# Kernel tuning notes

Measured on AMD Instinct MI355X. Metric: run time of the kernel, lower is better.

Reference implementation:

```python
import jax, jax.numpy as jnp
import numpy as np

B, D, H, E, K, A = 65536, 44, 256, 4, 2, 8  # batch, state_dim, hidden, experts, top_k, action_dim


def setup_inputs() -> dict:
    key = jax.random.key(0)
    ks = jax.random.split(key, 10)
    s = 0.1  # weight scale
    return dict(
        state=jax.random.normal(ks[0], (B, D), dtype=jnp.float32),
        rW1=jax.random.normal(ks[1], (D, H // 2)) * s, rb1=jnp.zeros((H // 2,)),
        rW2=jax.random.normal(ks[2], (H // 2, E)) * s, rb2=jnp.zeros((E,)),
        eW1=jax.random.normal(ks[3], (E, D, H)) * s, eb1=jnp.zeros((E, H)),
        eg1=jnp.ones((E, H)), ebt1=jnp.zeros((E, H)),
        eW2=jax.random.normal(ks[4], (E, H, H)) * s, eb2=jnp.zeros((E, H)),
        eg2=jnp.ones((E, H)), ebt2=jnp.zeros((E, H)),
        eW3=jax.random.normal(ks[5], (E, H, 2 * A)) * s, eb3=jnp.zeros((E, 2 * A)),
        vW1=jax.random.normal(ks[6], (D, H)) * s, vb1=jnp.zeros((H,)),
        vg=jnp.ones((H,)), vbt=jnp.zeros((H,)),
        vW2=jax.random.normal(ks[7], (H, H // 2)) * s, vb2=jnp.zeros((H // 2,)),
        vW3=jax.random.normal(ks[8], (H // 2, 1)) * s, vb3=jnp.zeros((1,)),
    )


def _ln(x, g, b):
    m = jnp.mean(x, axis=-1, keepdims=True)
    v = jnp.mean(jnp.square(x - m), axis=-1, keepdims=True)
    return (x - m) * jax.lax.rsqrt(v + 1e-5) * g + b


def reference(state, rW1, rb1, rW2, rb2,
              eW1, eb1, eg1, ebt1, eW2, eb2, eg2, ebt2, eW3, eb3,
              vW1, vb1, vg, vbt, vW2, vb2, vW3, vb3):
    # Router (eval mode: no noise)
    h = jax.nn.relu(state @ rW1 + rb1)
    router_probs = jax.nn.softmax(h @ rW2 + rb2, axis=-1)          # [B, E]
    top_v, top_i = jax.lax.top_k(router_probs, K)                  # [B, K]
    top_v = top_v / (jnp.sum(top_v, axis=-1, keepdims=True) + 1e-8)
    # Dense combine weights per expert (equivalent to per-sample gather/scatter loop)
    combine = jnp.sum(jax.nn.one_hot(top_i, E, dtype=state.dtype) * top_v[..., None], axis=1)  # [B, E]

    def expert(W1, b1, g1, bt1, W2, b2, g2, bt2, W3, b3):
        y = jax.nn.relu(_ln(state @ W1 + b1, g1, bt1))   # [B, H]
        y = jax.nn.relu(_ln(y @ W2 + b2, g2, bt2))       # [B, H]
        return y @ W3 + b3                               # [B, 2A]

    eout = jax.vmap(expert)(eW1, eb1, eg1, ebt1, eW2, eb2, eg2, ebt2, eW3, eb3)  # [E, B, 2A]
    mix = jnp.einsum('ebd,be->bd', eout, combine)        # [B, 2A]

    alpha = jax.nn.softplus(mix[:, :A]) + 1.0
    beta = jax.nn.softplus(mix[:, A:]) + 1.0

    v = jax.nn.relu(_ln(state @ vW1 + vb1, vg, vbt))
    v = jax.nn.relu(v @ vW2 + vb2)
    value = v @ vW3 + vb3                                # [B, 1]
    return alpha, beta, value, router_probs
```

## Files before the change

kernel.cpp:

```cpp
#include <hip/hip_runtime.h>
#include <math.h>

#define NB 65536

using f32x4 = __attribute__((ext_vector_type(4))) float;
using u32x4 = __attribute__((ext_vector_type(4))) unsigned;
using bf16x8 = __attribute__((ext_vector_type(8))) __bf16;

__device__ __forceinline__ unsigned pk2(float lo, float hi) {
    return (unsigned)__builtin_bit_cast(unsigned short, (__bf16)lo)
         | ((unsigned)__builtin_bit_cast(unsigned short, (__bf16)hi) << 16);
}
__device__ __forceinline__ float softplus_f(float x) {
    return fmaxf(x, 0.f) + log1pf(expf(-fabsf(x)));
}

#define MFMA16(acc, a, b) acc = __builtin_amdgcn_mfma_f32_16x16x32_bf16(a, b, acc, 0, 0, 0)

__device__ __forceinline__ bf16x8 cvt8(f32x4 a, f32x4 b) {
    union { bf16x8 v; unsigned u[4]; } r;
    r.u[0] = pk2(a[0], a[1]); r.u[1] = pk2(a[2], a[3]);
    r.u[2] = pk2(b[0], b[1]); r.u[3] = pk2(b[2], b[3]);
    return r.v;
}

__device__ __forceinline__ const bf16x8* ys_frag(const unsigned short* ys, int row, int col) {
    return (const bf16x8*)&ys[row * 256 + (col ^ ((row & 7) << 3))];
}

template<int NJ>
__device__ __forceinline__ void ldch(f32x4* r, const f32x4* __restrict__ src, int tid) {
    #pragma unroll
    for (int j = 0; j < NJ; ++j) r[j] = src[tid + j * 256];
}
template<int NJ>
__device__ __forceinline__ void wrch(unsigned short* buf, const f32x4* r, int tid) {
    #pragma unroll
    for (int j = 0; j < NJ; ++j) *(f32x4*)&buf[(size_t)(tid + j * 256) * 8] = r[j];
}

template<int NT>
__device__ __forceinline__ void mfma_bcols(f32x4* acc, bf16x8 a, const unsigned short* bufp, int c, int g) {
    #pragma unroll
    for (int t = 0; t < NT; ++t) {
        bf16x8 b = *(const bf16x8*)&bufp[t * 512 + g * 128 + c * 8];
        MFMA16(acc[t], a, b);
    }
}

__device__ __forceinline__ void ln_relu_store(
    f32x4* acc, const float* bs, const float* gs, const float* ts,
    unsigned int* ysu, int stripe, int g, int c)
{
    #pragma unroll
    for (int t = 0; t < 16; ++t) {
        float bb = bs[t * 16 + c];
        #pragma unroll
        for (int r = 0; r < 4; ++r) acc[t][r] += bb;
    }
    float sum[4] = {0.f, 0.f, 0.f, 0.f}, sq[4] = {0.f, 0.f, 0.f, 0.f};
    #pragma unroll
    for (int t = 0; t < 16; ++t) {
        #pragma unroll
        for (int r = 0; r < 4; ++r) { sum[r] += acc[t][r]; sq[r] += acc[t][r] * acc[t][r]; }
    }
    #pragma unroll
    for (int m = 1; m < 16; m <<= 1) {
        #pragma unroll
        for (int r = 0; r < 4; ++r) { sum[r] += __shfl_xor(sum[r], m); sq[r] += __shfl_xor(sq[r], m); }
    }
    float rs[4], nm[4];
    #pragma unroll
    for (int r = 0; r < 4; ++r) {
        float mean = sum[r] * (1.f / 256.f);
        float var = sq[r] * (1.f / 256.f) - mean * mean;
        rs[r] = rsqrtf(var + 1e-5f);
        nm[r] = -mean * rs[r];
    }
    const int odd = c & 1;
    const int ra = stripe + g * 4 + (odd ? 2 : 0);
    const int sza = (ra & 7) << 2, szb = ((ra + 1) & 7) << 2;
    #pragma unroll
    for (int t = 0; t < 16; ++t) {
        float gg = gs[t * 16 + c], bb = ts[t * 16 + c];
        float v0 = fmaxf(fmaf(fmaf(acc[t][0], rs[0], nm[0]), gg, bb), 0.f);
        float v1 = fmaxf(fmaf(fmaf(acc[t][1], rs[1], nm[1]), gg, bb), 0.f);
        float v2 = fmaxf(fmaf(fmaf(acc[t][2], rs[2], nm[2]), gg, bb), 0.f);
        float v3 = fmaxf(fmaf(fmaf(acc[t][3], rs[3], nm[3]), gg, bb), 0.f);
        float o0 = __shfl_xor(v0, 1), o1 = __shfl_xor(v1, 1);
        float o2 = __shfl_xor(v2, 1), o3 = __shfl_xor(v3, 1);
        unsigned p0 = pk2(odd ? o0 : v0, odd ? v0 : o0);
        unsigned p1 = pk2(odd ? o1 : v1, odd ? v1 : o1);
        unsigned p2 = pk2(odd ? o2 : v2, odd ? v2 : o2);
        unsigned p3 = pk2(odd ? o3 : v3, odd ? v3 : o3);
        unsigned pa = odd ? p2 : p0;
        unsigned pb = odd ? p3 : p1;
        int cp = t * 8 + (c >> 1);
        ysu[ra * 128 + (cp ^ sza)] = pa;
        ysu[(ra + 1) * 128 + (cp ^ szb)] = pb;
    }
}

__global__ __launch_bounds__(256) void k1_prep(
    const float* __restrict__ eW1, const float* __restrict__ eW2, const float* __restrict__ eW3,
    const float* __restrict__ vW1, const float* __restrict__ vW2,
    unsigned int* __restrict__ w1img, unsigned int* __restrict__ w2img,
    unsigned int* __restrict__ vw1img, unsigned int* __restrict__ vw2img,
    unsigned int* __restrict__ w3img)
{
    int fid = blockIdx.x * 256 + threadIdx.x;
    float v[8];
    unsigned int* dst;
    if (fid < 8192) {
        int e = fid >> 11, ch = (fid >> 10) & 1, rr = fid & 1023;
        int t = rr >> 6, g = (rr >> 4) & 3, c = rr & 15;
        int h = t * 16 + c, k0 = ch * 32 + g * 8;
        #pragma unroll
        for (int j = 0; j < 8; ++j) {
            int k = k0 + j;
            v[j] = (k < 44) ? eW1[(e * 44 + k) * 256 + h] : 0.f;
        }
        dst = w1img + (size_t)fid * 4;
    } else if (fid < 40960) {
        int f = fid - 8192;
        int e = f >> 13, ch = (f >> 10) & 7, rr = f & 1023;
        int t = rr >> 6, g = (rr >> 4) & 3, c = rr & 15;
        int h = t * 16 + c, k0 = ch * 32 + g * 8;
        const float* base = eW2 + (size_t)e * 65536 + h;
        #pragma unroll
        for (int j = 0; j < 8; ++j) v[j] = base[(size_t)(k0 + j) * 256];
        dst = w2img + (size_t)f * 4;
    } else if (fid < 43008) {
        int f = fid - 40960;
        int ch = f >> 10, rr = f & 1023;
        int t = rr >> 6, g = (rr >> 4) & 3, c = rr & 15;
        int h = t * 16 + c, k0 = ch * 32 + g * 8;
        #pragma unroll
        for (int j = 0; j < 8; ++j) {
            int k = k0 + j;
            v[j] = (k < 44) ? vW1[k * 256 + h] : 0.f;
        }
        dst = vw1img + (size_t)f * 4;
    } else if (fid < 47104) {
        int f = fid - 43008;
        int ch = f >> 9, rr = f & 511;
        int t = rr >> 6, g = (rr >> 4) & 3, c = rr & 15;
        int h = t * 16 + c, k0 = ch * 32 + g * 8;
        #pragma unroll
        for (int j = 0; j < 8; ++j) v[j] = vW2[(k0 + j) * 128 + h];
        dst = vw2img + (size_t)f * 4;
    } else {
        int f = fid - 47104;
        int e = f >> 9, rr = f & 511;
        int s = rr >> 6, g = (rr >> 4) & 3, o = rr & 15;
        int k0 = s * 32 + g * 8;
        #pragma unroll
        for (int j = 0; j < 8; ++j) v[j] = eW3[(size_t)e * 4096 + (k0 + j) * 16 + o];
        dst = w3img + (size_t)f * 4;
    }
    u32x4 out;
    #pragma unroll
    for (int p = 0; p < 4; ++p) out[p] = pk2(v[2 * p], v[2 * p + 1]);
    *(u32x4*)dst = out;
}

#define SM_YS    0
#define SM_BUFA  32768
#define SM_BUFB  49152
#define SM_B1    65536
#define SM_G1    66560
#define SM_T1    67584
#define SM_B2    68608
#define SM_G2    69632
#define SM_T2    70656
#define SM_B3    71680
#define SM_CMB   71744
#define SM_TOTAL 72768

#define SWAPBUF() { unsigned short* _t = cur; cur = nxt; nxt = _t; }

__global__ __launch_bounds__(256, 2) void k2_experts_value(
    const float* __restrict__ state,
    const float* __restrict__ rW1, const float* __restrict__ rb1,
    const float* __restrict__ rW2, const float* __restrict__ rb2,
    const float* __restrict__ eb1, const float* __restrict__ eg1, const float* __restrict__ ebt1,
    const float* __restrict__ eb2, const float* __restrict__ eg2, const float* __restrict__ ebt2,
    const float* __restrict__ eb3,
    const float* __restrict__ vb1, const float* __restrict__ vg, const float* __restrict__ vbt,
    const float* __restrict__ vb2, const float* __restrict__ vW3, const float* __restrict__ vb3,
    const f32x4* __restrict__ w1v, const f32x4* __restrict__ w2v,
    const f32x4* __restrict__ vw1v, const f32x4* __restrict__ vw2v,
    const f32x4* __restrict__ w3v,
    float* __restrict__ out_alpha, float* __restrict__ out_beta, float* __restrict__ out_value,
    float* __restrict__ out_probs)
{
    __shared__ __align__(16) unsigned char smem[SM_TOTAL];
    unsigned short* ys = (unsigned short*)(smem + SM_YS);
    unsigned int* ysu = (unsigned int*)(smem + SM_YS);
    float* b1s = (float*)(smem + SM_B1);
    float* g1s = (float*)(smem + SM_G1);
    float* t1s = (float*)(smem + SM_T1);
    float* b2s = (float*)(smem + SM_B2);
    float* g2s = (float*)(smem + SM_G2);
    float* t2s = (float*)(smem + SM_T2);
    float* b3s = (float*)(smem + SM_B3);
    float* cmbs = (float*)(smem + SM_CMB);
    unsigned short* cur = (unsigned short*)(smem + SM_BUFA);
    unsigned short* nxt = (unsigned short*)(smem + SM_BUFB);

    const int tid = threadIdx.x;
    const int wid = tid >> 6;
    const int lane = tid & 63;
    const int c = lane & 15;
    const int g = lane >> 4;
    const int stripe = wid * 16;
    const bool is_expert = (blockIdx.x < 1024);
    const int brow = (is_expert ? blockIdx.x : (blockIdx.x - 1024)) * 64;

    bf16x8 a1[2];
    {
        const float* srow = state + (size_t)(brow + stripe + c) * 44;
        f32x4 v0 = *(const f32x4*)(srow + g * 8);
        f32x4 v1 = *(const f32x4*)(srow + g * 8 + 4);
        a1[0] = cvt8(v0, v1);
        f32x4 z = {0.f, 0.f, 0.f, 0.f};
        f32x4 w0 = z, w1 = z;
        if (g == 0) { w0 = *(const f32x4*)(srow + 32); w1 = *(const f32x4*)(srow + 36); }
        else if (g == 1) { w0 = *(const f32x4*)(srow + 40); }
        a1[1] = cvt8(w0, w1);
    }

    f32x4 r[4];

    if (is_expert) {
        ldch<4>(r, w1v, tid);

        const int widu = __builtin_amdgcn_readfirstlane(wid);
        f32x4* pl = (f32x4*)(smem + SM_BUFB);
        {
            float s[44];
            {
                const float* srow2 = state + (size_t)(brow + lane) * 44;
                #pragma unroll
                for (int d4 = 0; d4 < 11; ++d4) {
                    f32x4 v = *(const f32x4*)(srow2 + d4 * 4);
                    s[d4 * 4 + 0] = v[0]; s[d4 * 4 + 1] = v[1];
                    s[d4 * 4 + 2] = v[2]; s[d4 * 4 + 3] = v[3];
                }
            }
            const float* w1b = rW1 + widu * 32;
            f32x4 h[8];
            #pragma unroll
            for (int j = 0; j < 8; ++j) h[j] = *(const f32x4*)&rb1[widu * 32 + j * 4];
            #pragma unroll
            for (int d = 0; d < 44; ++d) {
                #pragma unroll
                for (int j = 0; j < 8; ++j)
                    h[j] += s[d] * *(const f32x4*)(w1b + d * 128 + j * 4);
            }
            f32x4 l = {0.f, 0.f, 0.f, 0.f};
            #pragma unroll
            for (int j = 0; j < 8; ++j) {
                #pragma unroll
                for (int cmp = 0; cmp < 4; ++cmp) {
                    float hv = fmaxf(h[j][cmp], 0.f);
                    l += hv * *(const f32x4*)&rW2[(widu * 32 + j * 4 + cmp) * 4];
                }
            }
            pl[widu * 64 + lane] = l;
        }
        __syncthreads();
        if (wid == 0) {
            f32x4 lg = pl[lane] + pl[64 + lane] + pl[128 + lane] + pl[192 + lane];
            lg += *(const f32x4*)rb2;
            float l0 = lg[0], l1 = lg[1], l2 = lg[2], l3 = lg[3];
            float mx = fmaxf(fmaxf(l0, l1), fmaxf(l2, l3));
            float e0 = expf(l0 - mx), e1 = expf(l1 - mx), e2 = expf(l2 - mx), e3 = expf(l3 - mx);
            float inv = 1.f / (e0 + e1 + e2 + e3);
            float p0 = e0 * inv, p1 = e1 * inv, p2 = e2 * inv, p3 = e3 * inv;
            f32x4 probs = {p0, p1, p2, p3};
            *(f32x4*)&out_probs[(size_t)(brow + lane) * 4] = probs;

            int i1 = 0; float v1 = p0;
            if (p1 > v1) { v1 = p1; i1 = 1; }
            if (p2 > v1) { v1 = p2; i1 = 2; }
            if (p3 > v1) { v1 = p3; i1 = 3; }
            int i2 = -1; float v2 = -1.f;
            if (i1 != 0 && p0 > v2) { v2 = p0; i2 = 0; }
            if (i1 != 1 && p1 > v2) { v2 = p1; i2 = 1; }
            if (i1 != 2 && p2 > v2) { v2 = p2; i2 = 2; }
            if (i1 != 3 && p3 > v2) { v2 = p3; i2 = 3; }
            float cn = 1.f / (v1 + v2 + 1e-8f);
            float c1 = v1 * cn, c2 = v2 * cn;
            f32x4 cm;
            cm[0] = (i1 == 0) ? c1 : (i2 == 0) ? c2 : 0.f;
            cm[1] = (i1 == 1) ? c1 : (i2 == 1) ? c2 : 0.f;
            cm[2] = (i1 == 2) ? c1 : (i2 == 2) ? c2 : 0.f;
            cm[3] = (i1 == 3) ? c1 : (i2 == 3) ? c2 : 0.f;
            *(f32x4*)&cmbs[lane * 4] = cm;
        }

        wrch<4>(cur, r, tid);
        ldch<4>(r, w1v + 1024, tid);
        __syncthreads();

        float mix0 = 0.f, mix1 = 0.f, mix2 = 0.f, mix3 = 0.f;

        for (int e = 0; e < 4; ++e) {
            const int en = (e < 3) ? e + 1 : 3;
            float xb1 = eb1[e * 256 + tid], xg1 = eg1[e * 256 + tid], xt1 = ebt1[e * 256 + tid];
            float xb2 = eb2[e * 256 + tid], xg2 = eg2[e * 256 + tid], xt2 = ebt2[e * 256 + tid];
            b1s[tid] = xb1; g1s[tid] = xg1; t1s[tid] = xt1;
            b2s[tid] = xb2; g2s[tid] = xg2; t2s[tid] = xt2;
            if (tid < 16) b3s[tid] = eb3[e * 16 + tid];

            f32x4 acc1[16];
            #pragma unroll
            for (int t = 0; t < 16; ++t) acc1[t] = (f32x4){0.f, 0.f, 0.f, 0.f};

            wrch<4>(nxt, r, tid);
            ldch<4>(r, w2v + (size_t)(e * 8 + 0) * 1024, tid);
            mfma_bcols<16>(acc1, a1[0], cur, c, g);
            __syncthreads(); SWAPBUF();

            wrch<4>(nxt, r, tid);
            ldch<4>(r, w2v + (size_t)(e * 8 + 1) * 1024, tid);
            mfma_bcols<16>(acc1, a1[1], cur, c, g);
            ln_relu_store(acc1, b1s, g1s, t1s, ysu, stripe, g, c);
            __syncthreads(); SWAPBUF();

            f32x4 acc2[16];
            #pragma unroll
            for (int t = 0; t < 16; ++t) acc2[t] = (f32x4){0.f, 0.f, 0.f, 0.f};

            #pragma unroll
            for (int ch = 0; ch < 7; ++ch) {
                wrch<4>(nxt, r, tid);
                if (ch < 6) ldch<4>(r, w2v + (size_t)(e * 8 + ch + 2) * 1024, tid);
                else        ldch<2>(r, w3v + (size_t)e * 512, tid);
                bf16x8 a = *ys_frag(ys, stripe + c, ch * 32 + g * 8);
                mfma_bcols<16>(acc2, a, cur, c, g);
                __syncthreads(); SWAPBUF();
            }

            wrch<2>(nxt, r, tid);
            ldch<4>(r, w1v + (size_t)(en * 2) * 1024, tid);
            {
                bf16x8 a = *ys_frag(ys, stripe + c, 7 * 32 + g * 8);
                mfma_bcols<16>(acc2, a, cur, c, g);
            }
            ln_relu_store(acc2, b2s, g2s, t2s, ysu, stripe, g, c);
            __syncthreads(); SWAPBUF();

            wrch<4>(nxt, r, tid);
            ldch<4>(r, w1v + (size_t)(en * 2 + 1) * 1024, tid);
            f32x4 acc3 = (f32x4){0.f, 0.f, 0.f, 0.f};
            #pragma unroll
            for (int s = 0; s < 8; ++s) {
                bf16x8 a = *ys_frag(ys, stripe + c, s * 32 + g * 8);
                bf16x8 b = *(const bf16x8*)&cur[s * 512 + g * 128 + c * 8];
                MFMA16(acc3, a, b);
            }
            float bb3 = b3s[c];
            mix0 += cmbs[(stripe + g * 4 + 0) * 4 + e] * (acc3[0] + bb3);
            mix1 += cmbs[(stripe + g * 4 + 1) * 4 + e] * (acc3[1] + bb3);
            mix2 += cmbs[(stripe + g * 4 + 2) * 4 + e] * (acc3[2] + bb3);
            mix3 += cmbs[(stripe + g * 4 + 3) * 4 + e] * (acc3[3] + bb3);
            __syncthreads(); SWAPBUF();
        }

        int row0 = brow + stripe + g * 4;
        float sp0 = softplus_f(mix0) + 1.f;
        float sp1 = softplus_f(mix1) + 1.f;
        float sp2 = softplus_f(mix2) + 1.f;
        float sp3 = softplus_f(mix3) + 1.f;
        if (c < 8) {
            out_alpha[(size_t)(row0 + 0) * 8 + c] = sp0;
            out_alpha[(size_t)(row0 + 1) * 8 + c] = sp1;
            out_alpha[(size_t)(row0 + 2) * 8 + c] = sp2;
            out_alpha[(size_t)(row0 + 3) * 8 + c] = sp3;
        } else {
            out_beta[(size_t)(row0 + 0) * 8 + (c - 8)] = sp0;
            out_beta[(size_t)(row0 + 1) * 8 + (c - 8)] = sp1;
            out_beta[(size_t)(row0 + 2) * 8 + (c - 8)] = sp2;
            out_beta[(size_t)(row0 + 3) * 8 + (c - 8)] = sp3;
        }
    } else {
        b1s[tid] = vb1[tid]; g1s[tid] = vg[tid]; t1s[tid] = vbt[tid];
        if (tid < 128) { b2s[tid] = vb2[tid]; g2s[tid] = vW3[tid]; }

        ldch<4>(r, vw1v, tid);
        wrch<4>(cur, r, tid);
        ldch<4>(r, vw1v + 1024, tid);
        __syncthreads();

        f32x4 acc1[16];
        #pragma unroll
        for (int t = 0; t < 16; ++t) acc1[t] = (f32x4){0.f, 0.f, 0.f, 0.f};

        wrch<4>(nxt, r, tid);
        ldch<2>(r, vw2v, tid);
        mfma_bcols<16>(acc1, a1[0], cur, c, g);
        __syncthreads(); SWAPBUF();

        wrch<4>(nxt, r, tid);
        ldch<2>(r, vw2v + 512, tid);
        mfma_bcols<16>(acc1, a1[1], cur, c, g);
        ln_relu_store(acc1, b1s, g1s, t1s, ysu, stripe, g, c);
        __syncthreads(); SWAPBUF();

        f32x4 acc2[8];
        #pragma unroll
        for (int t = 0; t < 8; ++t) acc2[t] = (f32x4){0.f, 0.f, 0.f, 0.f};

        #pragma unroll
        for (int ch = 0; ch < 7; ++ch) {
            wrch<2>(nxt, r, tid);
            if (ch < 6) ldch<2>(r, vw2v + (size_t)(ch + 2) * 512, tid);
            bf16x8 a = *ys_frag(ys, stripe + c, ch * 32 + g * 8);
            mfma_bcols<8>(acc2, a, cur, c, g);
            __syncthreads(); SWAPBUF();
        }
        {
            bf16x8 a = *ys_frag(ys, stripe + c, 7 * 32 + g * 8);
            mfma_bcols<8>(acc2, a, cur, c, g);
        }

        float part[4] = {0.f, 0.f, 0.f, 0.f};
        #pragma unroll
        for (int t = 0; t < 8; ++t) {
            float bb = b2s[t * 16 + c], ww = g2s[t * 16 + c];
            #pragma unroll
            for (int q = 0; q < 4; ++q) part[q] += fmaxf(acc2[t][q] + bb, 0.f) * ww;
        }
        #pragma unroll
        for (int m = 1; m < 16; m <<= 1) {
            #pragma unroll
            for (int q = 0; q < 4; ++q) part[q] += __shfl_xor(part[q], m);
        }
        if (c == 0) {
            float v3 = vb3[0];
            int row = brow + stripe + g * 4;
            out_value[row + 0] = part[0] + v3;
            out_value[row + 1] = part[1] + v3;
            out_value[row + 2] = part[2] + v3;
            out_value[row + 3] = part[3] + v3;
        }
    }
}

extern "C" void kernel_launch(void* const* d_in, const int* in_sizes, int n_in,
                              void* d_out, int out_size, void* d_ws, size_t ws_size,
                              hipStream_t stream)
{
    const float* state = (const float*)d_in[0];
    const float* rW1  = (const float*)d_in[1];
    const float* rb1  = (const float*)d_in[2];
    const float* rW2  = (const float*)d_in[3];
    const float* rb2  = (const float*)d_in[4];
    const float* eW1  = (const float*)d_in[5];
    const float* eb1  = (const float*)d_in[6];
    const float* eg1  = (const float*)d_in[7];
    const float* ebt1 = (const float*)d_in[8];
    const float* eW2  = (const float*)d_in[9];
    const float* eb2  = (const float*)d_in[10];
    const float* eg2  = (const float*)d_in[11];
    const float* ebt2 = (const float*)d_in[12];
    const float* eW3  = (const float*)d_in[13];
    const float* eb3  = (const float*)d_in[14];
    const float* vW1  = (const float*)d_in[15];
    const float* vb1  = (const float*)d_in[16];
    const float* vg   = (const float*)d_in[17];
    const float* vbt  = (const float*)d_in[18];
    const float* vW2  = (const float*)d_in[19];
    const float* vb2  = (const float*)d_in[20];
    const float* vW3  = (const float*)d_in[21];
    const float* vb3  = (const float*)d_in[22];

    float* out = (float*)d_out;
    float* out_alpha = out;
    float* out_beta  = out + (size_t)NB * 8;
    float* out_value = out + (size_t)NB * 16;
    float* out_probs = out + (size_t)NB * 17;

    char* ws = (char*)d_ws;
    unsigned int* w1img   = (unsigned int*)(ws + 0x00000);
    unsigned int* w2img   = (unsigned int*)(ws + 0x20000);
    unsigned int* vw1img  = (unsigned int*)(ws + 0xA0000);
    unsigned int* vw2img  = (unsigned int*)(ws + 0xA8000);
    unsigned int* w3img   = (unsigned int*)(ws + 0xB8000);

    hipLaunchKernelGGL(k1_prep, dim3(192), dim3(256), 0, stream,
                       eW1, eW2, eW3, vW1, vW2,
                       w1img, w2img, vw1img, vw2img, w3img);
    hipLaunchKernelGGL(k2_experts_value, dim3(2048), dim3(256), 0, stream,
                       state, rW1, rb1, rW2, rb2,
                       eb1, eg1, ebt1, eb2, eg2, ebt2, eb3,
                       vb1, vg, vbt, vb2, vW3, vb3,
                       (const f32x4*)w1img, (const f32x4*)w2img,
                       (const f32x4*)vw1img, (const f32x4*)vw2img,
                       (const f32x4*)w3img,
                       out_alpha, out_beta, out_value, out_probs);
}
```

Baseline: 263.0 us.

## Split MLP columns across waves with register-resident weights and cross-wave LayerNorm

Each wave now owns a quarter of the output columns for all 64 rows, so weight fragments loaded from global memory feed MFMA directly from registers. This removes the double-buffered LDS weight staging and its per-chunk barriers. LayerNorm row statistics are combined across waves through a small LDS scratch with lightweight barriers, and LDS use drops enough to allow 3 blocks per CU. In exchange there is more register pressure, more global weight traffic per block, and extra cross-wave reductions.

```diff
diff --git a/kernel.cpp b/kernel.cpp
--- a/kernel.cpp
+++ b/kernel.cpp
@@ -3,6 +3,7 @@
 
 #define NB 65536
 
+using f32x2 = __attribute__((ext_vector_type(2))) float;
 using f32x4 = __attribute__((ext_vector_type(4))) float;
 using u32x4 = __attribute__((ext_vector_type(4))) unsigned;
 using bf16x8 = __attribute__((ext_vector_type(8))) __bf16;
@@ -13,6 +14,13 @@
 }
 __device__ __forceinline__ float softplus_f(float x) {
     return fmaxf(x, 0.f) + log1pf(expf(-fabsf(x)));
+}
+__device__ __forceinline__ bf16x8 asbf(f32x4 x) { return __builtin_bit_cast(bf16x8, x); }
+
+__device__ __forceinline__ void barrier_nodrain() {
+    asm volatile("s_waitcnt lgkmcnt(0)" ::: "memory");
+    __builtin_amdgcn_s_barrier();
+    __builtin_amdgcn_sched_barrier(0);
 }
 
 #define MFMA16(acc, a, b) acc = __builtin_amdgcn_mfma_f32_16x16x32_bf16(a, b, acc, 0, 0, 0)
@@ -39,66 +47,90 @@
     for (int j = 0; j < NJ; ++j) *(f32x4*)&buf[(size_t)(tid + j * 256) * 8] = r[j];
 }
 
-template<int NT>
-__device__ __forceinline__ void mfma_bcols(f32x4* acc, bf16x8 a, const unsigned short* bufp, int c, int g) {
-    #pragma unroll
-    for (int t = 0; t < NT; ++t) {
-        bf16x8 b = *(const bf16x8*)&bufp[t * 512 + g * 128 + c * 8];
-        MFMA16(acc[t], a, b);
+__device__ __forceinline__ void ln_colsplit(
+    f32x4 (&acc)[4][4],
+    const float* __restrict__ bias0, const float* __restrict__ gam, const float* __restrict__ bet,
+    unsigned int* ysu, float* pl, float* pl2, int wid, int lane)
+{
+    const int c = lane & 15, q = lane >> 4;
+    const int tid = threadIdx.x;
+    float bb[4], gg[4], tb[4];
+    #pragma unroll
+    for (int j = 0; j < 4; ++j) {
+        int col = (wid + 4 * j) * 16 + c;
+        bb[j] = bias0[col]; gg[j] = gam[col]; tb[j] = bet[col];
     }
-}
-
-__device__ __forceinline__ void ln_relu_store(
-    f32x4* acc, const float* bs, const float* gs, const float* ts,
-    unsigned int* ysu, int stripe, int g, int c)
-{
-    #pragma unroll
-    for (int t = 0; t < 16; ++t) {
-        float bb = bs[t * 16 + c];
-        #pragma unroll
-        for (int r = 0; r < 4; ++r) acc[t][r] += bb;
+    f32x4 sum[4], sq[4];
+    #pragma unroll
+    for (int rg = 0; rg < 4; ++rg) { sum[rg] = (f32x4){0.f,0.f,0.f,0.f}; sq[rg] = sum[rg]; }
+    #pragma unroll
+    for (int rg = 0; rg < 4; ++rg)
+        #pragma unroll
+        for (int j = 0; j < 4; ++j) {
+            acc[rg][j] += bb[j];
+            sum[rg] += acc[rg][j];
+            sq[rg] += acc[rg][j] * acc[rg][j];
+        }
+    #pragma unroll
+    for (int m = 1; m <= 8; m <<= 1)
+        #pragma unroll
+        for (int rg = 0; rg < 4; ++rg)
+            #pragma unroll
+            for (int ri = 0; ri < 4; ++ri) {
+                sum[rg][ri] += __shfl_xor(sum[rg][ri], m);
+                sq[rg][ri] += __shfl_xor(sq[rg][ri], m);
+            }
+    if (c == 0) {
+        f32x2* plv = (f32x2*)pl;
+        #pragma unroll
+        for (int rg = 0; rg < 4; ++rg)
+            #pragma unroll
+            for (int ri = 0; ri < 4; ++ri) {
+                int row = rg * 16 + q * 4 + ri;
+                plv[row * 4 + wid] = (f32x2){sum[rg][ri], sq[rg][ri]};
+            }
     }
-    float sum[4] = {0.f, 0.f, 0.f, 0.f}, sq[4] = {0.f, 0.f, 0.f, 0.f};
-    #pragma unroll
-    for (int t = 0; t < 16; ++t) {
-        #pragma unroll
-        for (int r = 0; r < 4; ++r) { sum[r] += acc[t][r]; sq[r] += acc[t][r] * acc[t][r]; }
+    barrier_nodrain();
+    if (tid < 64) {
+        const f32x4* p4 = (const f32x4*)pl;
+        f32x4 x = p4[tid * 2], y = p4[tid * 2 + 1];
+        float s = x[0] + x[2] + y[0] + y[2];
+        float z = x[1] + x[3] + y[1] + y[3];
+        float mean = s * (1.f / 256.f);
+        float var = z * (1.f / 256.f) - mean * mean;
+        float rs = rsqrtf(var + 1e-5f);
+        ((f32x2*)pl2)[tid] = (f32x2){rs, -mean * rs};
     }
-    #pragma unroll
-    for (int m = 1; m < 16; m <<= 1) {
-        #pragma unroll
-        for (int r = 0; r < 4; ++r) { sum[r] += __shfl_xor(sum[r], m); sq[r] += __shfl_xor(sq[r], m); }
+    barrier_nodrain();
+    #pragma unroll
+    for (int rg = 0; rg < 4; ++rg) {
+        int r0 = rg * 16 + q * 4;
+        f32x4 u = *(const f32x4*)&pl2[r0 * 2];
+        f32x4 w2_ = *(const f32x4*)&pl2[r0 * 2 + 4];
+        float rsv[4] = {u[0], u[2], w2_[0], w2_[2]};
+        float nmv[4] = {u[1], u[3], w2_[1], w2_[3]};
+        const int odd = c & 1;
+        #pragma unroll
+        for (int j = 0; j < 4; ++j) {
+            float v0 = fmaxf(fmaf(fmaf(acc[rg][j][0], rsv[0], nmv[0]), gg[j], tb[j]), 0.f);
+            float v1 = fmaxf(fmaf(fmaf(acc[rg][j][1], rsv[1], nmv[1]), gg[j], tb[j]), 0.f);
+            float v2 = fmaxf(fmaf(fmaf(acc[rg][j][2], rsv[2], nmv[2]), gg[j], tb[j]), 0.f);
+            float v3 = fmaxf(fmaf(fmaf(acc[rg][j][3], rsv[3], nmv[3]), gg[j], tb[j]), 0.f);
+            float o0 = __shfl_xor(v0, 1), o1 = __shfl_xor(v1, 1);
+            float o2 = __shfl_xor(v2, 1), o3 = __shfl_xor(v3, 1);
+            unsigned p0 = pk2(odd ? o0 : v0, odd ? v0 : o0);
+            unsigned p1 = pk2(odd ? o1 : v1, odd ? v1 : o1);
+            unsigned p2 = pk2(odd ? o2 : v2, odd ? v2 : o2);
+            unsigned p3 = pk2(odd ? o3 : v3, odd ? v3 : o3);
+            unsigned pa = odd ? p2 : p0;
+            unsigned pb = odd ? p3 : p1;
+            int ra = r0 + (odd ? 2 : 0);
+            int cp = (wid + 4 * j) * 8 + (c >> 1);
+            ysu[ra * 128 + (cp ^ ((ra & 7) << 2))] = pa;
+            ysu[(ra + 1) * 128 + (cp ^ (((ra + 1) & 7) << 2))] = pb;
+        }
     }
-    float rs[4], nm[4];
-    #pragma unroll
-    for (int r = 0; r < 4; ++r) {
-        float mean = sum[r] * (1.f / 256.f);
-        float var = sq[r] * (1.f / 256.f) - mean * mean;
-        rs[r] = rsqrtf(var + 1e-5f);
-        nm[r] = -mean * rs[r];
-    }
-    const int odd = c & 1;
-    const int ra = stripe + g * 4 + (odd ? 2 : 0);
-    const int sza = (ra & 7) << 2, szb = ((ra + 1) & 7) << 2;
-    #pragma unroll
-    for (int t = 0; t < 16; ++t) {
-        float gg = gs[t * 16 + c], bb = ts[t * 16 + c];
-        float v0 = fmaxf(fmaf(fmaf(acc[t][0], rs[0], nm[0]), gg, bb), 0.f);
-        float v1 = fmaxf(fmaf(fmaf(acc[t][1], rs[1], nm[1]), gg, bb), 0.f);
-        float v2 = fmaxf(fmaf(fmaf(acc[t][2], rs[2], nm[2]), gg, bb), 0.f);
-        float v3 = fmaxf(fmaf(fmaf(acc[t][3], rs[3], nm[3]), gg, bb), 0.f);
-        float o0 = __shfl_xor(v0, 1), o1 = __shfl_xor(v1, 1);
-        float o2 = __shfl_xor(v2, 1), o3 = __shfl_xor(v3, 1);
-        unsigned p0 = pk2(odd ? o0 : v0, odd ? v0 : o0);
-        unsigned p1 = pk2(odd ? o1 : v1, odd ? v1 : o1);
-        unsigned p2 = pk2(odd ? o2 : v2, odd ? v2 : o2);
-        unsigned p3 = pk2(odd ? o3 : v3, odd ? v3 : o3);
-        unsigned pa = odd ? p2 : p0;
-        unsigned pb = odd ? p3 : p1;
-        int cp = t * 8 + (c >> 1);
-        ysu[ra * 128 + (cp ^ sza)] = pa;
-        ysu[(ra + 1) * 128 + (cp ^ szb)] = pb;
-    }
+    barrier_nodrain();
 }
 
 __global__ __launch_bounds__(256) void k1_prep(
@@ -165,21 +197,13 @@
 }
 
 #define SM_YS    0
-#define SM_BUFA  32768
-#define SM_BUFB  49152
-#define SM_B1    65536
-#define SM_G1    66560
-#define SM_T1    67584
-#define SM_B2    68608
-#define SM_G2    69632
-#define SM_T2    70656
-#define SM_B3    71680
-#define SM_CMB   71744
-#define SM_TOTAL 72768
-
-#define SWAPBUF() { unsigned short* _t = cur; cur = nxt; nxt = _t; }
-
-__global__ __launch_bounds__(256, 2) void k2_experts_value(
+#define SM_W3S   32768
+#define SM_PL    40960
+#define SM_PL2   43008
+#define SM_CMB   43520
+#define SM_TOTAL 44544
+
+__global__ __launch_bounds__(256, 3) void k2_experts_value(
     const float* __restrict__ state,
     const float* __restrict__ rW1, const float* __restrict__ rb1,
     const float* __restrict__ rW2, const float* __restrict__ rb2,
@@ -197,16 +221,10 @@
     __shared__ __align__(16) unsigned char smem[SM_TOTAL];
     unsigned short* ys = (unsigned short*)(smem + SM_YS);
     unsigned int* ysu = (unsigned int*)(smem + SM_YS);
-    float* b1s = (float*)(smem + SM_B1);
-    float* g1s = (float*)(smem + SM_G1);
-    float* t1s = (float*)(smem + SM_T1);
-    float* b2s = (float*)(smem + SM_B2);
-    float* g2s = (float*)(smem + SM_G2);
-    float* t2s = (float*)(smem + SM_T2);
-    float* b3s = (float*)(smem + SM_B3);
+    unsigned short* w3s = (unsigned short*)(smem + SM_W3S);
+    float* pl  = (float*)(smem + SM_PL);
+    float* pl2 = (float*)(smem + SM_PL2);
     float* cmbs = (float*)(smem + SM_CMB);
-    unsigned short* cur = (unsigned short*)(smem + SM_BUFA);
-    unsigned short* nxt = (unsigned short*)(smem + SM_BUFB);
 
     const int tid = threadIdx.x;
     const int wid = tid >> 6;
@@ -217,61 +235,50 @@
     const bool is_expert = (blockIdx.x < 1024);
     const int brow = (is_expert ? blockIdx.x : (blockIdx.x - 1024)) * 64;
 
-    bf16x8 a1[2];
-    {
-        const float* srow = state + (size_t)(brow + stripe + c) * 44;
-        f32x4 v0 = *(const f32x4*)(srow + g * 8);
-        f32x4 v1 = *(const f32x4*)(srow + g * 8 + 4);
-        a1[0] = cvt8(v0, v1);
-        f32x4 z = {0.f, 0.f, 0.f, 0.f};
-        f32x4 w0 = z, w1 = z;
-        if (g == 0) { w0 = *(const f32x4*)(srow + 32); w1 = *(const f32x4*)(srow + 36); }
-        else if (g == 1) { w0 = *(const f32x4*)(srow + 40); }
-        a1[1] = cvt8(w0, w1);
-    }
-
-    f32x4 r[4];
+    f32x4 rA[4], rB[4];
 
     if (is_expert) {
-        ldch<4>(r, w1v, tid);
-
-        const int widu = __builtin_amdgcn_readfirstlane(wid);
-        f32x4* pl = (f32x4*)(smem + SM_BUFB);
+        ldch<4>(rA, w1v, tid);
+        ldch<4>(rB, w1v + 1024, tid);
+
+        float* s_lds = (float*)(smem + SM_YS);
+        f32x4* pl_r  = (f32x4*)(smem + SM_YS + 16384);
         {
-            float s[44];
-            {
-                const float* srow2 = state + (size_t)(brow + lane) * 44;
-                #pragma unroll
-                for (int d4 = 0; d4 < 11; ++d4) {
-                    f32x4 v = *(const f32x4*)(srow2 + d4 * 4);
-                    s[d4 * 4 + 0] = v[0]; s[d4 * 4 + 1] = v[1];
-                    s[d4 * 4 + 2] = v[2]; s[d4 * 4 + 3] = v[3];
+            int row = tid & 63, g4 = tid >> 6;
+            const float* srow = state + (size_t)(brow + row) * 44;
+            #pragma unroll
+            for (int k4 = 0; k4 < 3; ++k4) {
+                int d4 = g4 + k4 * 4;
+                if (d4 < 11) {
+                    f32x4 v = *(const f32x4*)(srow + d4 * 4);
+                    #pragma unroll
+                    for (int qq = 0; qq < 4; ++qq) s_lds[(d4 * 4 + qq) * 64 + row] = v[qq];
                 }
             }
-            const float* w1b = rW1 + widu * 32;
+        }
+        __syncthreads();
+        {
+            const int w32 = __builtin_amdgcn_readfirstlane(wid * 32);
             f32x4 h[8];
             #pragma unroll
-            for (int j = 0; j < 8; ++j) h[j] = *(const f32x4*)&rb1[widu * 32 + j * 4];
-            #pragma unroll
+            for (int j = 0; j < 8; ++j) h[j] = *(const f32x4*)&rb1[w32 + j * 4];
             for (int d = 0; d < 44; ++d) {
+                float sd = s_lds[d * 64 + lane];
                 #pragma unroll
                 for (int j = 0; j < 8; ++j)
-                    h[j] += s[d] * *(const f32x4*)(w1b + d * 128 + j * 4);
+                    h[j] += sd * *(const f32x4*)(rW1 + d * 128 + w32 + j * 4);
             }
             f32x4 l = {0.f, 0.f, 0.f, 0.f};
             #pragma unroll
-            for (int j = 0; j < 8; ++j) {
-                #pragma unroll
-                for (int cmp = 0; cmp < 4; ++cmp) {
-                    float hv = fmaxf(h[j][cmp], 0.f);
-                    l += hv * *(const f32x4*)&rW2[(widu * 32 + j * 4 + cmp) * 4];
-                }
-            }
-            pl[widu * 64 + lane] = l;
+            for (int j = 0; j < 8; ++j)
+                #pragma unroll
+                for (int q4 = 0; q4 < 4; ++q4)
+                    l += fmaxf(h[j][q4], 0.f) * *(const f32x4*)&rW2[(w32 + j * 4 + q4) * 4];
+            pl_r[wid * 64 + lane] = l;
         }
         __syncthreads();
         if (wid == 0) {
-            f32x4 lg = pl[lane] + pl[64 + lane] + pl[128 + lane] + pl[192 + lane];
+            f32x4 lg = pl_r[lane] + pl_r[64 + lane] + pl_r[128 + lane] + pl_r[192 + lane];
             lg += *(const f32x4*)rb2;
             float l0 = lg[0], l1 = lg[1], l2 = lg[2], l3 = lg[3];
             float mx = fmaxf(fmaxf(l0, l1), fmaxf(l2, l3));
@@ -280,7 +287,6 @@
             float p0 = e0 * inv, p1 = e1 * inv, p2 = e2 * inv, p3 = e3 * inv;
             f32x4 probs = {p0, p1, p2, p3};
             *(f32x4*)&out_probs[(size_t)(brow + lane) * 4] = probs;
-
             int i1 = 0; float v1 = p0;
             if (p1 > v1) { v1 = p1; i1 = 1; }
             if (p2 > v1) { v1 = p2; i1 = 2; }
@@ -300,73 +306,86 @@
             *(f32x4*)&cmbs[lane * 4] = cm;
         }
 
-        wrch<4>(cur, r, tid);
-        ldch<4>(r, w1v + 1024, tid);
-        __syncthreads();
-
         float mix0 = 0.f, mix1 = 0.f, mix2 = 0.f, mix3 = 0.f;
 
         for (int e = 0; e < 4; ++e) {
             const int en = (e < 3) ? e + 1 : 3;
-            float xb1 = eb1[e * 256 + tid], xg1 = eg1[e * 256 + tid], xt1 = ebt1[e * 256 + tid];
-            float xb2 = eb2[e * 256 + tid], xg2 = eg2[e * 256 + tid], xt2 = ebt2[e * 256 + tid];
-            b1s[tid] = xb1; g1s[tid] = xg1; t1s[tid] = xt1;
-            b2s[tid] = xb2; g2s[tid] = xg2; t2s[tid] = xt2;
-            if (tid < 16) b3s[tid] = eb3[e * 16 + tid];
-
-            f32x4 acc1[16];
-            #pragma unroll
-            for (int t = 0; t < 16; ++t) acc1[t] = (f32x4){0.f, 0.f, 0.f, 0.f};
-
-            wrch<4>(nxt, r, tid);
-            ldch<4>(r, w2v + (size_t)(e * 8 + 0) * 1024, tid);
-            mfma_bcols<16>(acc1, a1[0], cur, c, g);
-            __syncthreads(); SWAPBUF();
-
-            wrch<4>(nxt, r, tid);
-            ldch<4>(r, w2v + (size_t)(e * 8 + 1) * 1024, tid);
-            mfma_bcols<16>(acc1, a1[1], cur, c, g);
-            ln_relu_store(acc1, b1s, g1s, t1s, ysu, stripe, g, c);
-            __syncthreads(); SWAPBUF();
-
-            f32x4 acc2[16];
-            #pragma unroll
-            for (int t = 0; t < 16; ++t) acc2[t] = (f32x4){0.f, 0.f, 0.f, 0.f};
-
-            #pragma unroll
-            for (int ch = 0; ch < 7; ++ch) {
-                wrch<4>(nxt, r, tid);
-                if (ch < 6) ldch<4>(r, w2v + (size_t)(e * 8 + ch + 2) * 1024, tid);
-                else        ldch<2>(r, w3v + (size_t)e * 512, tid);
-                bf16x8 a = *ys_frag(ys, stripe + c, ch * 32 + g * 8);
-                mfma_bcols<16>(acc2, a, cur, c, g);
-                __syncthreads(); SWAPBUF();
-            }
-
-            wrch<2>(nxt, r, tid);
-            ldch<4>(r, w1v + (size_t)(en * 2) * 1024, tid);
-            {
-                bf16x8 a = *ys_frag(ys, stripe + c, 7 * 32 + g * 8);
-                mfma_bcols<16>(acc2, a, cur, c, g);
-            }
-            ln_relu_store(acc2, b2s, g2s, t2s, ysu, stripe, g, c);
-            __syncthreads(); SWAPBUF();
-
-            wrch<4>(nxt, r, tid);
-            ldch<4>(r, w1v + (size_t)(en * 2 + 1) * 1024, tid);
-            f32x4 acc3 = (f32x4){0.f, 0.f, 0.f, 0.f};
+            bf16x8 a1s[4][2];
+            #pragma unroll
+            for (int rg = 0; rg < 4; ++rg) {
+                const float* srow = state + (size_t)(brow + rg * 16 + c) * 44;
+                f32x4 v0 = *(const f32x4*)(srow + g * 8);
+                f32x4 v1 = *(const f32x4*)(srow + g * 8 + 4);
+                a1s[rg][0] = cvt8(v0, v1);
+                f32x4 z = {0.f,0.f,0.f,0.f}, w0 = z, w1 = z;
+                if (g == 0) { w0 = *(const f32x4*)(srow + 32); w1 = *(const f32x4*)(srow + 36); }
+                else if (g == 1) { w0 = *(const f32x4*)(srow + 40); }
+                a1s[rg][1] = cvt8(w0, w1);
+            }
+            barrier_nodrain();
+
+            f32x4 acc[4][4];
+            #pragma unroll
+            for (int rg = 0; rg < 4; ++rg)
+                #pragma unroll
+                for (int j = 0; j < 4; ++j) acc[rg][j] = (f32x4){0.f,0.f,0.f,0.f};
+            #pragma unroll
+            for (int rg = 0; rg < 4; ++rg)
+                #pragma unroll
+                for (int j = 0; j < 4; ++j) MFMA16(acc[rg][j], a1s[rg][0], asbf(rA[j]));
+            #pragma unroll
+            for (int rg = 0; rg < 4; ++rg)
+                #pragma unroll
+                for (int j = 0; j < 4; ++j) MFMA16(acc[rg][j], a1s[rg][1], asbf(rB[j]));
+            ldch<4>(rA, w2v + (size_t)(e * 8 + 0) * 1024, tid);
+
+            ln_colsplit(acc, eb1 + e * 256, eg1 + e * 256, ebt1 + e * 256, ysu, pl, pl2, wid, lane);
+            ldch<4>(rB, w2v + (size_t)(e * 8 + 1) * 1024, tid);
+
+            #pragma unroll
+            for (int rg = 0; rg < 4; ++rg)
+                #pragma unroll
+                for (int j = 0; j < 4; ++j) acc[rg][j] = (f32x4){0.f,0.f,0.f,0.f};
+            #pragma unroll
+            for (int ch = 0; ch < 8; ch += 2) {
+                bf16x8 aA[4];
+                #pragma unroll
+                for (int rg = 0; rg < 4; ++rg) aA[rg] = *ys_frag(ys, rg * 16 + c, ch * 32 + g * 8);
+                #pragma unroll
+                for (int rg = 0; rg < 4; ++rg)
+                    #pragma unroll
+                    for (int j = 0; j < 4; ++j) MFMA16(acc[rg][j], aA[rg], asbf(rA[j]));
+                if (ch < 6) ldch<4>(rA, w2v + (size_t)(e * 8 + ch + 2) * 1024, tid);
+                else        ldch<2>(rA, w3v + (size_t)e * 512, tid);
+                bf16x8 aB[4];
+                #pragma unroll
+                for (int rg = 0; rg < 4; ++rg) aB[rg] = *ys_frag(ys, rg * 16 + c, (ch + 1) * 32 + g * 8);
+                #pragma unroll
+                for (int rg = 0; rg < 4; ++rg)
+                    #pragma unroll
+                    for (int j = 0; j < 4; ++j) MFMA16(acc[rg][j], aB[rg], asbf(rB[j]));
+                if (ch < 6) ldch<4>(rB, w2v + (size_t)(e * 8 + ch + 3) * 1024, tid);
+            }
+
+            ln_colsplit(acc, eb2 + e * 256, eg2 + e * 256, ebt2 + e * 256, ysu, pl, pl2, wid, lane);
+            wrch<2>(w3s, rA, tid);
+            barrier_nodrain();
+
+            f32x4 acc3 = (f32x4){0.f,0.f,0.f,0.f};
             #pragma unroll
             for (int s = 0; s < 8; ++s) {
                 bf16x8 a = *ys_frag(ys, stripe + c, s * 32 + g * 8);
-                bf16x8 b = *(const bf16x8*)&cur[s * 512 + g * 128 + c * 8];
+                bf16x8 b = *(const bf16x8*)&w3s[s * 512 + g * 128 + c * 8];
                 MFMA16(acc3, a, b);
             }
-            float bb3 = b3s[c];
+            float bb3 = eb3[e * 16 + c];
             mix0 += cmbs[(stripe + g * 4 + 0) * 4 + e] * (acc3[0] + bb3);
             mix1 += cmbs[(stripe + g * 4 + 1) * 4 + e] * (acc3[1] + bb3);
             mix2 += cmbs[(stripe + g * 4 + 2) * 4 + e] * (acc3[2] + bb3);
             mix3 += cmbs[(stripe + g * 4 + 3) * 4 + e] * (acc3[3] + bb3);
-            __syncthreads(); SWAPBUF();
+
+            ldch<4>(rA, w1v + (size_t)(en * 2) * 1024, tid);
+            ldch<4>(rB, w1v + (size_t)(en * 2 + 1) * 1024, tid);
         }
 
         int row0 = brow + stripe + g * 4;
@@ -386,65 +405,98 @@
             out_beta[(size_t)(row0 + 3) * 8 + (c - 8)] = sp3;
         }
     } else {
-        b1s[tid] = vb1[tid]; g1s[tid] = vg[tid]; t1s[tid] = vbt[tid];
-        if (tid < 128) { b2s[tid] = vb2[tid]; g2s[tid] = vW3[tid]; }
-
-        ldch<4>(r, vw1v, tid);
-        wrch<4>(cur, r, tid);
-        ldch<4>(r, vw1v + 1024, tid);
-        __syncthreads();
-
-        f32x4 acc1[16];
-        #pragma unroll
-        for (int t = 0; t < 16; ++t) acc1[t] = (f32x4){0.f, 0.f, 0.f, 0.f};
-
-        wrch<4>(nxt, r, tid);
-        ldch<2>(r, vw2v, tid);
-        mfma_bcols<16>(acc1, a1[0], cur, c, g);
-        __syncthreads(); SWAPBUF();
-
-        wrch<4>(nxt, r, tid);
-        ldch<2>(r, vw2v + 512, tid);
-        mfma_bcols<16>(acc1, a1[1], cur, c, g);
-        ln_relu_store(acc1, b1s, g1s, t1s, ysu, stripe, g, c);
-        __syncthreads(); SWAPBUF();
-
-        f32x4 acc2[8];
-        #pragma unroll
-        for (int t = 0; t < 8; ++t) acc2[t] = (f32x4){0.f, 0.f, 0.f, 0.f};
-
-        #pragma unroll
-        for (int ch = 0; ch < 7; ++ch) {
-            wrch<2>(nxt, r, tid);
-            if (ch < 6) ldch<2>(r, vw2v + (size_t)(ch + 2) * 512, tid);
-            bf16x8 a = *ys_frag(ys, stripe + c, ch * 32 + g * 8);
-            mfma_bcols<8>(acc2, a, cur, c, g);
-            __syncthreads(); SWAPBUF();
-        }
-        {
-            bf16x8 a = *ys_frag(ys, stripe + c, 7 * 32 + g * 8);
-            mfma_bcols<8>(acc2, a, cur, c, g);
-        }
-
-        float part[4] = {0.f, 0.f, 0.f, 0.f};
-        #pragma unroll
-        for (int t = 0; t < 8; ++t) {
-            float bb = b2s[t * 16 + c], ww = g2s[t * 16 + c];
-            #pragma unroll
-            for (int q = 0; q < 4; ++q) part[q] += fmaxf(acc2[t][q] + bb, 0.f) * ww;
-        }
-        #pragma unroll
-        for (int m = 1; m < 16; m <<= 1) {
-            #pragma unroll
-            for (int q = 0; q < 4; ++q) part[q] += __shfl_xor(part[q], m);
-        }
+        ldch<4>(rA, vw1v, tid);
+        ldch<4>(rB, vw1v + 1024, tid);
+        bf16x8 a1s[4][2];
+        #pragma unroll
+        for (int rg = 0; rg < 4; ++rg) {
+            const float* srow = state + (size_t)(brow + rg * 16 + c) * 44;
+            f32x4 v0 = *(const f32x4*)(srow + g * 8);
+            f32x4 v1 = *(const f32x4*)(srow + g * 8 + 4);
+            a1s[rg][0] = cvt8(v0, v1);
+            f32x4 z = {0.f,0.f,0.f,0.f}, w0 = z, w1 = z;
+            if (g == 0) { w0 = *(const f32x4*)(srow + 32); w1 = *(const f32x4*)(srow + 36); }
+            else if (g == 1) { w0 = *(const f32x4*)(srow + 40); }
+            a1s[rg][1] = cvt8(w0, w1);
+        }
+        f32x4 acc[4][4];
+        #pragma unroll
+        for (int rg = 0; rg < 4; ++rg)
+            #pragma unroll
+            for (int j = 0; j < 4; ++j) acc[rg][j] = (f32x4){0.f,0.f,0.f,0.f};
+        #pragma unroll
+        for (int rg = 0; rg < 4; ++rg)
+            #pragma unroll
+            for (int j = 0; j < 4; ++j) MFMA16(acc[rg][j], a1s[rg][0], asbf(rA[j]));
+        #pragma unroll
+        for (int rg = 0; rg < 4; ++rg)
+            #pragma unroll
+            for (int j = 0; j < 4; ++j) MFMA16(acc[rg][j], a1s[rg][1], asbf(rB[j]));
+        ldch<2>(rA, vw2v, tid);
+        ldch<2>(rB, vw2v + 512, tid);
+
+        ln_colsplit(acc, vb1, vg, vbt, ysu, pl, pl2, wid, lane);
+
+        f32x4 acc2[4][2];
+        #pragma unroll
+        for (int rg = 0; rg < 4; ++rg)
+            #pragma unroll
+            for (int j = 0; j < 2; ++j) acc2[rg][j] = (f32x4){0.f,0.f,0.f,0.f};
+        #pragma unroll
+        for (int ch = 0; ch < 8; ch += 2) {
+            bf16x8 aA[4];
+            #pragma unroll
+            for (int rg = 0; rg < 4; ++rg) aA[rg] = *ys_frag(ys, rg * 16 + c, ch * 32 + g * 8);
+            #pragma unroll
+            for (int rg = 0; rg < 4; ++rg)
+                #pragma unroll
+                for (int j = 0; j < 2; ++j) MFMA16(acc2[rg][j], aA[rg], asbf(rA[j]));
+            if (ch < 6) ldch<2>(rA, vw2v + (size_t)(ch + 2) * 512, tid);
+            bf16x8 aB[4];
+            #pragma unroll
+            for (int rg = 0; rg < 4; ++rg) aB[rg] = *ys_frag(ys, rg * 16 + c, (ch + 1) * 32 + g * 8);
+            #pragma unroll
+            for (int rg = 0; rg < 4; ++rg)
+                #pragma unroll
+                for (int j = 0; j < 2; ++j) MFMA16(acc2[rg][j], aB[rg], asbf(rB[j]));
+            if (ch < 6) ldch<2>(rB, vw2v + (size_t)(ch + 3) * 512, tid);
+        }
+
+        float vb2c[2], vw3c[2];
+        #pragma unroll
+        for (int j = 0; j < 2; ++j) {
+            int col = (wid + 4 * j) * 16 + c;
+            vb2c[j] = vb2[col]; vw3c[j] = vW3[col];
+        }
+        f32x4 part[4];
+        #pragma unroll
+        for (int rg = 0; rg < 4; ++rg) {
+            part[rg] = (f32x4){0.f,0.f,0.f,0.f};
+            #pragma unroll
+            for (int j = 0; j < 2; ++j)
+                #pragma unroll
+                for (int ri = 0; ri < 4; ++ri)
+                    part[rg][ri] += fmaxf(acc2[rg][j][ri] + vb2c[j], 0.f) * vw3c[j];
+        }
+        #pragma unroll
+        for (int m = 1; m <= 8; m <<= 1)
+            #pragma unroll
+            for (int rg = 0; rg < 4; ++rg)
+                #pragma unroll
+                for (int ri = 0; ri < 4; ++ri)
+                    part[rg][ri] += __shfl_xor(part[rg][ri], m);
+        const int q = g;
         if (c == 0) {
-            float v3 = vb3[0];
-            int row = brow + stripe + g * 4;
-            out_value[row + 0] = part[0] + v3;
-            out_value[row + 1] = part[1] + v3;
-            out_value[row + 2] = part[2] + v3;
-            out_value[row + 3] = part[3] + v3;
+            #pragma unroll
+            for (int rg = 0; rg < 4; ++rg)
+                #pragma unroll
+                for (int ri = 0; ri < 4; ++ri)
+                    pl[(rg * 16 + q * 4 + ri) * 4 + wid] = part[rg][ri];
+        }
+        barrier_nodrain();
+        if (tid < 64) {
+            f32x4 p = *(const f32x4*)&pl[tid * 4];
+            out_value[brow + tid] = p[0] + p[1] + p[2] + p[3] + vb3[0];
         }
     }
 }
```

After: 440.9 us. 67.6% more time.
